# Kernel optimization log

Measured on AMD Instinct MI355X. Metric: run time of the kernel, lower is better.

Reference implementation:

```python
import jax, jax.numpy as jnp
import numpy as np

N_NODES = 100000
N_EDGES = 3200000
IN_DIM, HID, N_LAB = 128, 64, 121


def setup_inputs() -> dict:
    key = jax.random.key(0)
    ks = jax.random.split(key, 8)
    x = jax.random.normal(ks[0], (N_NODES, IN_DIM), dtype=jnp.float32)
    edge_index = jax.random.randint(ks[1], (2, N_EDGES), 0, N_NODES, dtype=jnp.int64)
    W1 = jax.random.normal(ks[2], (IN_DIM, HID), dtype=jnp.float32) * (1.0 / np.sqrt(IN_DIM))
    b1 = jnp.zeros((HID,), dtype=jnp.float32)
    W2 = jax.random.normal(ks[3], (HID, HID), dtype=jnp.float32) * (1.0 / np.sqrt(HID))
    b2 = jnp.zeros((HID,), dtype=jnp.float32)
    Wout = jax.random.normal(ks[4], (HID, N_LAB), dtype=jnp.float32) * (1.0 / np.sqrt(HID))
    bout = jnp.zeros((N_LAB,), dtype=jnp.float32)
    return {"x": x, "edge_index": edge_index, "W1": W1, "b1": b1,
            "W2": W2, "b2": b2, "Wout": Wout, "bout": bout}


def _gcn_conv(x, W, b, src, dst, norm, n):
    # x' = D^{-1/2}(A+I)D^{-1/2} X W + b  (edges already include self-loops)
    xw = x @ W                                   # [N, out]
    msg = xw[src] * norm[:, None]                # [E+N, out] gather + scale
    agg = jax.ops.segment_sum(msg, dst, num_segments=n)  # scatter-add
    return agg + b


def reference(x, edge_index, W1, b1, W2, b2, Wout, bout):
    n = x.shape[0]
    loop = jnp.arange(n, dtype=edge_index.dtype)
    src = jnp.concatenate([edge_index[0], loop])
    dst = jnp.concatenate([edge_index[1], loop])
    # symmetric normalization (self-loops guarantee deg >= 1)
    deg = jax.ops.segment_sum(jnp.ones_like(dst, dtype=x.dtype), dst, num_segments=n)
    dinv = jax.lax.rsqrt(deg)
    norm = dinv[src] * dinv[dst]                 # [E+N]

    h = jax.nn.relu(_gcn_conv(x, W1, b1, src, dst, norm, n))
    # dropout p=0.5 is identity in eval mode (training=False)
    h = jax.nn.relu(_gcn_conv(h, W2, b2, src, dst, norm, n))
    logits = h @ Wout + bout                     # [N, num_labels]
    return logits
```

## Files before the change

### kernel.cpp

```cpp
#include <hip/hip_runtime.h>
#include <hip/hip_bf16.h>
#include <hip/hip_fp16.h>


#define IN_DIM 128
#define HID 64
#define N_LAB 121
#define NB_BLK 256

__global__ void scan1(const int* __restrict__ in, int* __restrict__ out,
                      int* __restrict__ bsums, int n) {
    __shared__ int s[256];
    int i = blockIdx.x * 256 + threadIdx.x;
    int v = (i < n) ? in[i] : 0;
    s[threadIdx.x] = v;
    __syncthreads();
    for (int off = 1; off < 256; off <<= 1) {
        int t = (threadIdx.x >= off) ? s[threadIdx.x - off] : 0;
        __syncthreads();
        s[threadIdx.x] += t;
        __syncthreads();
    }
    if (i < n) out[i] = s[threadIdx.x] - v;
    if (threadIdx.x == 255) bsums[blockIdx.x] = s[255];
}

__global__ void scan2(int* __restrict__ bsums, int nb) {
    __shared__ int s[512];
    int v = (threadIdx.x < nb) ? bsums[threadIdx.x] : 0;
    s[threadIdx.x] = v;
    __syncthreads();
    for (int off = 1; off < 512; off <<= 1) {
        int t = (threadIdx.x >= off) ? s[threadIdx.x - off] : 0;
        __syncthreads();
        s[threadIdx.x] += t;
        __syncthreads();
    }
    if (threadIdx.x < nb) bsums[threadIdx.x] = s[threadIdx.x] - v;
}

__global__ void scan_add(int* __restrict__ out, const int* __restrict__ bsums, int n) {
    int i = blockIdx.x * 256 + threadIdx.x;
    if (i < n) out[i] += bsums[blockIdx.x];
}

__global__ __launch_bounds__(256) void bucket_count(const int* __restrict__ dst,
                                                    int* __restrict__ counts,
                                                    int nbuk, int chunk, int E) {
    extern __shared__ int c[];
    for (int j = threadIdx.x; j < nbuk; j += 256) c[j] = 0;
    __syncthreads();
    int beg = blockIdx.x * chunk;
    int end = min(beg + chunk, E);
    for (int i = beg + threadIdx.x; i < end; i += 256)
        atomicAdd(&c[dst[i] >> 8], 1);
    __syncthreads();
    for (int j = threadIdx.x; j < nbuk; j += 256)
        counts[j * NB_BLK + blockIdx.x] = c[j];
}

__global__ __launch_bounds__(256) void bucket_scatter(const int* __restrict__ src,
                                                      const int* __restrict__ dst,
                                                      const int* __restrict__ base,
                                                      int* __restrict__ bucketed,
                                                      int nbuk, int chunk, int E) {
    extern __shared__ int c[];
    for (int j = threadIdx.x; j < nbuk; j += 256) c[j] = 0;
    __syncthreads();
    int beg = blockIdx.x * chunk;
    int end = min(beg + chunk, E);
    for (int i = beg + threadIdx.x; i < end; i += 256) {
        int d = dst[i];
        int b = d >> 8;
        int r = atomicAdd(&c[b], 1);
        int pos = base[b * NB_BLK + blockIdx.x] + r;
        bucketed[pos] = ((d & 255) << 17) | src[i];
    }
}

__global__ __launch_bounds__(256) void bucket_sort(const int* __restrict__ bucketed,
                                                   const int* __restrict__ base,
                                                   int* __restrict__ srcs,
                                                   int* __restrict__ row_ptr,
                                                   float* __restrict__ dinv,
                                                   int nbuk, int N, int E) {
    __shared__ int h[256];
    __shared__ int cur[256];
    int b = blockIdx.x;
    int nodeBase = b << 8;
    int s = base[b * NB_BLK];
    int e = (b == nbuk - 1) ? E : base[(b + 1) * NB_BLK];
    h[threadIdx.x] = 0;
    __syncthreads();
    for (int i = s + threadIdx.x; i < e; i += 256)
        atomicAdd(&h[bucketed[i] >> 17], 1);
    __syncthreads();
    int v = h[threadIdx.x];
    for (int off = 1; off < 256; off <<= 1) {
        int t = (threadIdx.x >= off) ? h[threadIdx.x - off] : 0;
        __syncthreads();
        h[threadIdx.x] += t;
        __syncthreads();
    }
    int excl = h[threadIdx.x] - v;
    cur[threadIdx.x] = excl;
    int node = nodeBase + threadIdx.x;
    if (node < N) {
        row_ptr[node] = s + excl;
        dinv[node] = rsqrtf((float)v + 1.0f);
    }
    if (b == nbuk - 1 && threadIdx.x == 0) row_ptr[N] = E;
    __syncthreads();
    for (int i = s + threadIdx.x; i < e; i += 256) {
        int p = bucketed[i];
        int d = p >> 17;
        int r = atomicAdd(&cur[d], 1);
        srcs[s + r] = p & 0x1FFFF;
    }
}

template <int K, int N, typename OT>
__global__ __launch_bounds__(256) void gemm_kernel(
        const float* __restrict__ A, const float* __restrict__ B,
        const float* __restrict__ bias, const float* __restrict__ rowscale,
        OT* __restrict__ C, int M) {
    constexpr int ROWS = 64;
    constexpr int NPAD = (N <= 64) ? 64 : 128;
    constexpr int CG = NPAD / 4;
    constexpr int RG = 256 / CG;
    constexpr int RPT = ROWS / RG;
    __shared__ float Bs[K * NPAD];
    __shared__ float As[ROWS * K];

    for (int i = threadIdx.x; i < K * NPAD; i += 256) {
        int c = i & (NPAD - 1);
        int k = i / NPAD;
        Bs[i] = (c < N) ? B[k * N + c] : 0.f;
    }
    const int row_base = blockIdx.x * ROWS;
    const float* Ablk = A + (size_t)row_base * K;
    int avail = (M - row_base) * K;
    if (avail > ROWS * K) avail = ROWS * K;
    const int nvec = avail >> 2;
    const float4* __restrict__ Av = (const float4*)Ablk;
    float4* Asv = (float4*)As;
    for (int i = threadIdx.x; i < nvec; i += 256) Asv[i] = Av[i];
    __syncthreads();

    const int cg = threadIdx.x % CG;
    const int rg = threadIdx.x / CG;

    float acc[RPT][4];
    #pragma unroll
    for (int j = 0; j < RPT; ++j) {
        acc[j][0] = 0.f; acc[j][1] = 0.f; acc[j][2] = 0.f; acc[j][3] = 0.f;
    }

    for (int k = 0; k < K; k += 4) {
        float4 Bq[4];
        #pragma unroll
        for (int kk = 0; kk < 4; ++kk)
            Bq[kk] = *(const float4*)&Bs[(k + kk) * NPAD + cg * 4];
        #pragma unroll
        for (int j = 0; j < RPT; ++j) {
            const float4 Aq = *(const float4*)&As[(rg + RG * j) * K + k];
            #pragma unroll
            for (int c = 0; c < 4; ++c) {
                const float b0 = ((const float*)&Bq[0])[c];
                const float b1 = ((const float*)&Bq[1])[c];
                const float b2 = ((const float*)&Bq[2])[c];
                const float b3 = ((const float*)&Bq[3])[c];
                float a = acc[j][c];
                a = fmaf(Aq.x, b0, a);
                a = fmaf(Aq.y, b1, a);
                a = fmaf(Aq.z, b2, a);
                a = fmaf(Aq.w, b3, a);
                acc[j][c] = a;
            }
        }
    }

    float bv[4];
    #pragma unroll
    for (int c = 0; c < 4; ++c) {
        int col = cg * 4 + c;
        bv[c] = (bias && col < N) ? bias[col] : 0.f;
    }

    #pragma unroll
    for (int j = 0; j < RPT; ++j) {
        const int r = row_base + rg + RG * j;
        if (r >= M) continue;
        const float sc = rowscale ? rowscale[r] : 1.0f;
        float o[4];
        #pragma unroll
        for (int c = 0; c < 4; ++c) o[c] = fmaf(acc[j][c], sc, bv[c]);
        OT* Crow = C + (size_t)r * N;
        if constexpr (sizeof(OT) == 4 && (N % 4 == 0)) {
            *(float4*)&Crow[cg * 4] = make_float4(o[0], o[1], o[2], o[3]);
        } else if constexpr (sizeof(OT) == 2 && (N % 4 == 0)) {
            __half2* p = (__half2*)&Crow[cg * 4];
            p[0] = __floats2half2_rn(o[0], o[1]);
            p[1] = __floats2half2_rn(o[2], o[3]);
        } else {
            #pragma unroll
            for (int c = 0; c < 4; ++c) {
                int col = cg * 4 + c;
                if (col < N) Crow[col] = (OT)o[c];
            }
        }
    }
}

__global__ __launch_bounds__(256) void aggregate(
        const __half* __restrict__ feat2, const int* __restrict__ rp,
        const int* __restrict__ srcs, const float* __restrict__ dinv,
        const float* __restrict__ bias, float* __restrict__ out, int N) {
    const int wid = (int)((((size_t)blockIdx.x * 256) + threadIdx.x) >> 6);
    if (wid >= N) return;
    const int lane = threadIdx.x & 63;
    const int slot = lane >> 3;
    const int oct  = lane & 7;
    const size_t fbase = (size_t)oct << 3;

    float acc[8];
    #pragma unroll
    for (int i = 0; i < 8; ++i) acc[i] = 0.f;

    if (slot == 0) {
        const uint4 raw = *(const uint4*)(feat2 + (((size_t)wid << 6) + fbase));
        const __half2* h = (const __half2*)&raw;
        #pragma unroll
        for (int i = 0; i < 4; ++i) {
            const float2 f = __half22float2(h[i]);
            acc[2 * i]     += f.x;
            acc[2 * i + 1] += f.y;
        }
    }

    const int beg = rp[wid], end = rp[wid + 1];
    int e = beg;
    for (; e + 16 <= end; e += 16) {
        const int s0 = srcs[e + slot];
        const int s1 = srcs[e + 8 + slot];
        const uint4 r0 = *(const uint4*)(feat2 + (((size_t)s0 << 6) + fbase));
        const uint4 r1 = *(const uint4*)(feat2 + (((size_t)s1 << 6) + fbase));
        const __half2* h0 = (const __half2*)&r0;
        const __half2* h1 = (const __half2*)&r1;
        #pragma unroll
        for (int i = 0; i < 4; ++i) {
            const float2 f0 = __half22float2(h0[i]);
            const float2 f1 = __half22float2(h1[i]);
            acc[2 * i]     += f0.x + f1.x;
            acc[2 * i + 1] += f0.y + f1.y;
        }
    }
    for (; e < end; e += 8) {
        const int idx = e + slot;
        if (idx < end) {
            const int s = srcs[idx];
            const uint4 r0 = *(const uint4*)(feat2 + (((size_t)s << 6) + fbase));
            const __half2* h0 = (const __half2*)&r0;
            #pragma unroll
            for (int i = 0; i < 4; ++i) {
                const float2 f = __half22float2(h0[i]);
                acc[2 * i]     += f.x;
                acc[2 * i + 1] += f.y;
            }
        }
    }

    #pragma unroll
    for (int m = 8; m <= 32; m <<= 1) {
        #pragma unroll
        for (int i = 0; i < 8; ++i)
            acc[i] += __shfl_xor(acc[i], m, 64);
    }

    if (slot == 0) {
        const float sc = dinv[wid];
        float o[8];
        #pragma unroll
        for (int i = 0; i < 8; ++i)
            o[i] = fmaxf(fmaf(acc[i], sc, bias[fbase + i]), 0.f);
        float4* dst4 = (float4*)(out + (((size_t)wid << 6) + fbase));
        dst4[0] = make_float4(o[0], o[1], o[2], o[3]);
        dst4[1] = make_float4(o[4], o[5], o[6], o[7]);
    }
}

extern "C" void kernel_launch(void* const* d_in, const int* in_sizes, int n_in,
                              void* d_out, int out_size, void* d_ws, size_t ws_size,
                              hipStream_t stream) {
    const float* x    = (const float*)d_in[0];
    const int*   ei   = (const int*)d_in[1];
    const float* W1   = (const float*)d_in[2];
    const float* b1   = (const float*)d_in[3];
    const float* W2   = (const float*)d_in[4];
    const float* b2   = (const float*)d_in[5];
    const float* Wout = (const float*)d_in[6];
    const float* bout = (const float*)d_in[7];
    float* out = (float*)d_out;

    const int N = in_sizes[0] / IN_DIM;
    const int E = in_sizes[1] / 2;
    const int* srcI = ei;
    const int* dstI = ei + E;

    const int nbuk = (N + 255) >> 8;
    const int M1 = nbuk * NB_BLK;
    const int chunk = (E + NB_BLK - 1) / NB_BLK;

    int*    row_ptr = (int*)d_ws;
    float*  dinv    = (float*)(row_ptr + (N + 1));
    int*    counts  = (int*)(dinv + N);
    int*    base    = counts + M1;
    int*    bsums2  = base + M1;
    int*    srcs    = bsums2 + 512;
    __half* feat2   = (__half*)(((uintptr_t)(srcs + E) + 15) & ~(uintptr_t)15);
    float*  hbuf    = (float*)(feat2 + (size_t)N * HID);
    int*    bucketed = (int*)feat2;

    const int nbM = (M1 + 255) / 256;
    const int gemmBlocks = (N + 63) / 64;
    const int aggBlocks = (int)(((size_t)N * HID + 255) / 256);
    const size_t ldsBuk = (size_t)nbuk * sizeof(int);

    bucket_count<<<NB_BLK, 256, ldsBuk, stream>>>(dstI, counts, nbuk, chunk, E);
    scan1<<<nbM, 256, 0, stream>>>(counts, base, bsums2, M1);
    scan2<<<1, 512, 0, stream>>>(bsums2, nbM);
    scan_add<<<nbM, 256, 0, stream>>>(base, bsums2, M1);
    bucket_scatter<<<NB_BLK, 256, ldsBuk, stream>>>(srcI, dstI, base, bucketed, nbuk, chunk, E);
    bucket_sort<<<nbuk, 256, 0, stream>>>(bucketed, base, srcs, row_ptr, dinv, nbuk, N, E);

    gemm_kernel<IN_DIM, HID, __half><<<gemmBlocks, 256, 0, stream>>>(x, W1, nullptr, dinv, feat2, N);
    aggregate<<<aggBlocks, 256, 0, stream>>>(feat2, row_ptr, srcs, dinv, b1, hbuf, N);

    gemm_kernel<HID, HID, __half><<<gemmBlocks, 256, 0, stream>>>(hbuf, W2, nullptr, dinv, feat2, N);
    aggregate<<<aggBlocks, 256, 0, stream>>>(feat2, row_ptr, srcs, dinv, b2, hbuf, N);

    gemm_kernel<HID, N_LAB, float><<<gemmBlocks, 256, 0, stream>>>(hbuf, Wout, bout, nullptr, out, N);
}
```

Before: 522.7 us.

## Store GCN features in 16-column planes and aggregate per feature chunk

The first two GEMMs now write their half-precision output as four planar 16-column slabs instead of row-major 64-wide rows. Aggregation is split by feature chunk: each block handles one chunk for 16 rows, four rows per wavefront, and lanes gather 32-byte segments. Each slab is N*16 halves (about 3.2 MB), so the gather working set per chunk is more likely to stay in cache. In exchange, every edge index is read four times, row-pointer loads are repeated, and each gather moves only 32 bytes, which risks more instruction and index-load overhead. The loop over edges also drops the unroll by two.

After: 547.4 us. 4.7% more time.

```diff
diff --git a/kernel.cpp b/kernel.cpp
--- a/kernel.cpp
+++ b/kernel.cpp
@@ -7,6 +7,8 @@
 #define HID 64
 #define N_LAB 121
 #define NB_BLK 256
+#define FCHUNK 16
+#define NCHUNK (HID / FCHUNK)
 
 __global__ void scan1(const int* __restrict__ in, int* __restrict__ out,
                       int* __restrict__ bsums, int n) {
@@ -119,7 +121,7 @@
     }
 }
 
-template <int K, int N, typename OT>
+template <int K, int N, typename OT, bool PLANAR>
 __global__ __launch_bounds__(256) void gemm_kernel(
         const float* __restrict__ A, const float* __restrict__ B,
         const float* __restrict__ bias, const float* __restrict__ rowscale,
@@ -195,41 +197,56 @@
         float o[4];
         #pragma unroll
         for (int c = 0; c < 4; ++c) o[c] = fmaf(acc[j][c], sc, bv[c]);
-        OT* Crow = C + (size_t)r * N;
-        if constexpr (sizeof(OT) == 4 && (N % 4 == 0)) {
-            *(float4*)&Crow[cg * 4] = make_float4(o[0], o[1], o[2], o[3]);
-        } else if constexpr (sizeof(OT) == 2 && (N % 4 == 0)) {
-            __half2* p = (__half2*)&Crow[cg * 4];
-            p[0] = __floats2half2_rn(o[0], o[1]);
-            p[1] = __floats2half2_rn(o[2], o[3]);
+        if constexpr (PLANAR) {
+            const int plane = (cg * 4) >> 4;
+            const int incol = (cg * 4) & 15;
+            __half* Cp = (__half*)C + (size_t)plane * ((size_t)M * FCHUNK)
+                       + (size_t)r * FCHUNK + incol;
+            ((__half2*)Cp)[0] = __floats2half2_rn(o[0], o[1]);
+            ((__half2*)Cp)[1] = __floats2half2_rn(o[2], o[3]);
         } else {
-            #pragma unroll
-            for (int c = 0; c < 4; ++c) {
-                int col = cg * 4 + c;
-                if (col < N) Crow[col] = (OT)o[c];
+            OT* Crow = C + (size_t)r * N;
+            if constexpr (sizeof(OT) == 4 && (N % 4 == 0)) {
+                *(float4*)&Crow[cg * 4] = make_float4(o[0], o[1], o[2], o[3]);
+            } else if constexpr (sizeof(OT) == 2 && (N % 4 == 0)) {
+                __half2* p = (__half2*)&Crow[cg * 4];
+                p[0] = __floats2half2_rn(o[0], o[1]);
+                p[1] = __floats2half2_rn(o[2], o[3]);
+            } else {
+                #pragma unroll
+                for (int c = 0; c < 4; ++c) {
+                    int col = cg * 4 + c;
+                    if (col < N) Crow[col] = (OT)o[c];
+                }
             }
         }
     }
 }
 
-__global__ __launch_bounds__(256) void aggregate(
-        const __half* __restrict__ feat2, const int* __restrict__ rp,
+__global__ __launch_bounds__(256) void aggregate_chunked(
+        const __half* __restrict__ feat2p, const int* __restrict__ rp,
         const int* __restrict__ srcs, const float* __restrict__ dinv,
-        const float* __restrict__ bias, float* __restrict__ out, int N) {
-    const int wid = (int)((((size_t)blockIdx.x * 256) + threadIdx.x) >> 6);
-    if (wid >= N) return;
-    const int lane = threadIdx.x & 63;
-    const int slot = lane >> 3;
-    const int oct  = lane & 7;
-    const size_t fbase = (size_t)oct << 3;
+        const float* __restrict__ bias, float* __restrict__ out,
+        int N, int bpc) {
+    const int chunk = blockIdx.x / bpc;
+    const int rb    = blockIdx.x % bpc;
+    const int lane  = threadIdx.x & 63;
+    const int wv    = threadIdx.x >> 6;
+    const int rloc  = lane >> 4;
+    const int slot  = (lane >> 1) & 7;
+    const int oct   = lane & 1;
+    const int row   = rb * 16 + wv * 4 + rloc;
+    const bool rowok = (row < N);
+
+    const __half* fb = feat2p + (size_t)chunk * ((size_t)N * FCHUNK) + oct * 8;
 
     float acc[8];
     #pragma unroll
     for (int i = 0; i < 8; ++i) acc[i] = 0.f;
 
-    if (slot == 0) {
-        const uint4 raw = *(const uint4*)(feat2 + (((size_t)wid << 6) + fbase));
-        const __half2* h = (const __half2*)&raw;
+    if (slot == 0 && rowok) {
+        const uint4 q = *(const uint4*)(fb + (size_t)row * FCHUNK);
+        const __half2* h = (const __half2*)&q;
         #pragma unroll
         for (int i = 0; i < 4; ++i) {
             const float2 f = __half22float2(h[i]);
@@ -238,54 +255,41 @@
         }
     }
 
-    const int beg = rp[wid], end = rp[wid + 1];
-    int e = beg;
-    for (; e + 16 <= end; e += 16) {
-        const int s0 = srcs[e + slot];
-        const int s1 = srcs[e + 8 + slot];
-        const uint4 r0 = *(const uint4*)(feat2 + (((size_t)s0 << 6) + fbase));
-        const uint4 r1 = *(const uint4*)(feat2 + (((size_t)s1 << 6) + fbase));
-        const __half2* h0 = (const __half2*)&r0;
-        const __half2* h1 = (const __half2*)&r1;
-        #pragma unroll
-        for (int i = 0; i < 4; ++i) {
-            const float2 f0 = __half22float2(h0[i]);
-            const float2 f1 = __half22float2(h1[i]);
-            acc[2 * i]     += f0.x + f1.x;
-            acc[2 * i + 1] += f0.y + f1.y;
-        }
-    }
-    for (; e < end; e += 8) {
-        const int idx = e + slot;
+    const int beg = rowok ? rp[row] : 0;
+    const int end = rowok ? rp[row + 1] : 0;
+    int idx = beg + slot;
+    while (__any(idx < end)) {
         if (idx < end) {
             const int s = srcs[idx];
-            const uint4 r0 = *(const uint4*)(feat2 + (((size_t)s << 6) + fbase));
-            const __half2* h0 = (const __half2*)&r0;
+            const uint4 q = *(const uint4*)(fb + (size_t)s * FCHUNK);
+            const __half2* h = (const __half2*)&q;
             #pragma unroll
             for (int i = 0; i < 4; ++i) {
-                const float2 f = __half22float2(h0[i]);
+                const float2 f = __half22float2(h[i]);
                 acc[2 * i]     += f.x;
                 acc[2 * i + 1] += f.y;
             }
         }
-    }
-
-    #pragma unroll
-    for (int m = 8; m <= 32; m <<= 1) {
+        idx += 8;
+    }
+
+    #pragma unroll
+    for (int m = 2; m <= 8; m <<= 1) {
         #pragma unroll
         for (int i = 0; i < 8; ++i)
             acc[i] += __shfl_xor(acc[i], m, 64);
     }
 
-    if (slot == 0) {
-        const float sc = dinv[wid];
+    if ((lane & 14) == 0 && rowok) {
+        const float sc = dinv[row];
+        const int cf = chunk * FCHUNK + oct * 8;
         float o[8];
         #pragma unroll
         for (int i = 0; i < 8; ++i)
-            o[i] = fmaxf(fmaf(acc[i], sc, bias[fbase + i]), 0.f);
-        float4* dst4 = (float4*)(out + (((size_t)wid << 6) + fbase));
-        dst4[0] = make_float4(o[0], o[1], o[2], o[3]);
-        dst4[1] = make_float4(o[4], o[5], o[6], o[7]);
+            o[i] = fmaxf(fmaf(acc[i], sc, bias[cf + i]), 0.f);
+        float4* d4 = (float4*)(out + (size_t)row * HID + cf);
+        d4[0] = make_float4(o[0], o[1], o[2], o[3]);
+        d4[1] = make_float4(o[4], o[5], o[6], o[7]);
     }
 }
 
@@ -323,7 +327,8 @@
 
     const int nbM = (M1 + 255) / 256;
     const int gemmBlocks = (N + 63) / 64;
-    const int aggBlocks = (int)(((size_t)N * HID + 255) / 256);
+    const int bpc = (N + 15) / 16;
+    const int aggBlocks = NCHUNK * bpc;
     const size_t ldsBuk = (size_t)nbuk * sizeof(int);
 
     bucket_count<<<NB_BLK, 256, ldsBuk, stream>>>(dstI, counts, nbuk, chunk, E);
@@ -333,11 +338,11 @@
     bucket_scatter<<<NB_BLK, 256, ldsBuk, stream>>>(srcI, dstI, base, bucketed, nbuk, chunk, E);
     bucket_sort<<<nbuk, 256, 0, stream>>>(bucketed, base, srcs, row_ptr, dinv, nbuk, N, E);
 
-    gemm_kernel<IN_DIM, HID, __half><<<gemmBlocks, 256, 0, stream>>>(x, W1, nullptr, dinv, feat2, N);
-    aggregate<<<aggBlocks, 256, 0, stream>>>(feat2, row_ptr, srcs, dinv, b1, hbuf, N);
-
-    gemm_kernel<HID, HID, __half><<<gemmBlocks, 256, 0, stream>>>(hbuf, W2, nullptr, dinv, feat2, N);
-    aggregate<<<aggBlocks, 256, 0, stream>>>(feat2, row_ptr, srcs, dinv, b2, hbuf, N);
-
-    gemm_kernel<HID, N_LAB, float><<<gemmBlocks, 256, 0, stream>>>(hbuf, Wout, bout, nullptr, out, N);
-}
+    gemm_kernel<IN_DIM, HID, __half, true><<<gemmBlocks, 256, 0, stream>>>(x, W1, nullptr, dinv, feat2, N);
+    aggregate_chunked<<<aggBlocks, 256, 0, stream>>>(feat2, row_ptr, srcs, dinv, b1, hbuf, N, bpc);
+
+    gemm_kernel<HID, HID, __half, true><<<gemmBlocks, 256, 0, stream>>>(hbuf, W2, nullptr, dinv, feat2, N);
+    aggregate_chunked<<<aggBlocks, 256, 0, stream>>>(feat2, row_ptr, srcs, dinv, b2, hbuf, N, bpc);
+
+    gemm_kernel<HID, N_LAB, float, false><<<gemmBlocks, 256, 0, stream>>>(hbuf, Wout, bout, nullptr, out, N);
+}
```
